# Kernel optimization log

Measured on AMD Instinct MI355X. Metric: run time of the kernel, lower is better.

The kernel has to match this reference:

```python
import jax, jax.numpy as jnp
import numpy as np

N, D, K = 32768, 256, 8192
SQRT3 = 3.0 ** 0.5


def setup_inputs() -> dict:
    key = jax.random.key(0)
    k1, k2 = jax.random.split(key)
    x = jax.random.normal(k1, (N, D), dtype=jnp.float32)
    # torch .uniform_(-sqrt(3), sqrt(3)) on an [D, K] table
    embeddings = jax.random.uniform(k2, (D, K), dtype=jnp.float32,
                                    minval=-SQRT3, maxval=SQRT3)
    return {"x": x, "embeddings": embeddings}


def reference(x, embeddings):
    # x: [N, D] (forward flattens from dim 1; 2D input is identity)
    # embeddings: [D, K]
    # squared L2 distances: ||y||^2 - 2 y.E + ||e||^2  -> [N, K]
    dist = (jnp.sum(x * x, axis=1, keepdims=True)
            - 2.0 * (x @ embeddings)
            + jnp.sum(embeddings * embeddings, axis=0, keepdims=True))
    idx = jnp.argmin(dist, axis=1)  # [N]
    # one_hot(idx) @ E^T == gather of columns of E (same math, no dense one-hot)
    quantized = jnp.take(embeddings, idx, axis=1).T  # [N, D]
    return quantized.reshape(x.shape)
```

## Files before the change

kernel.cpp:

```cpp
#include <hip/hip_runtime.h>
#include <math.h>
#include <float.h>

#define N_ROWS 32768
#define D_DIM  256
#define K_DIM  8192

#define EPS1 0.25f
#define EPS2 0.02f
#define T2CAP 4096
#define T3CAP 512
#define NSPLIT3 16

typedef _Float16 f16;
typedef _Float16 f16x8 __attribute__((ext_vector_type(8)));
typedef float f32x4 __attribute__((ext_vector_type(4)));

#define KSPLIT 8
#define COLS_PER_SPLIT (K_DIM / KSPLIT)
#define CHUNK_COLS 32
#define NCHUNK (COLS_PER_SPLIT / CHUNK_COLS)
#define CHUNK_BYTES (CHUNK_COLS * D_DIM * 2)

typedef unsigned int u32;
typedef const u32 __attribute__((address_space(1)))* gas1_u32;
typedef u32 __attribute__((address_space(3)))* las3_u32;
__device__ __forceinline__ void gload_lds16(const void* g, void* l) {
    __builtin_amdgcn_global_load_lds((gas1_u32)g, (las3_u32)l, 16, 0, 0);
}

__global__ void convx_kernel(const float* __restrict__ X, f16* __restrict__ X16) {
    const size_t i = ((size_t)blockIdx.x * 256 + threadIdx.x) * 8;
    float4 a = *reinterpret_cast<const float4*>(X + i);
    float4 b = *reinterpret_cast<const float4*>(X + i + 4);
    f16x8 o;
    o[0]=(f16)a.x; o[1]=(f16)a.y; o[2]=(f16)a.z; o[3]=(f16)a.w;
    o[4]=(f16)b.x; o[5]=(f16)b.y; o[6]=(f16)b.z; o[7]=(f16)b.w;
    *reinterpret_cast<f16x8*>(X16 + i) = o;
}

__global__ void transpose_kernel(const float* __restrict__ E, float* __restrict__ ET) {
    __shared__ float t[64][65];
    const int bk = blockIdx.x & (K_DIM / 64 - 1);
    const int bd = blockIdx.x >> 7;
    const int c  = threadIdx.x & 63;
    const int r0 = (threadIdx.x >> 6) * 16;
    const int d0 = bd * 64, k0 = bk * 64;
#pragma unroll
    for (int i = 0; i < 16; ++i)
        t[r0 + i][c] = E[(size_t)(d0 + r0 + i) * K_DIM + k0 + c];
    __syncthreads();
#pragma unroll
    for (int i = 0; i < 16; ++i)
        ET[(size_t)(k0 + r0 + i) * D_DIM + d0 + c] = t[c][r0 + i];
}

__global__ void packe_et_kernel(const float* __restrict__ ET, f16* __restrict__ Epack) {
    const int gid = blockIdx.x * 256 + threadIdx.x;
    const int l    = gid & 63;
    const int t    = (gid >> 6) & 7;
    const int tile = gid >> 9;
    const int k  = 16 * tile + (l & 15);
    const int d0 = 32 * t + (l >> 4) * 8;
    float4 a = *reinterpret_cast<const float4*>(&ET[(size_t)k * D_DIM + d0]);
    float4 b = *reinterpret_cast<const float4*>(&ET[(size_t)k * D_DIM + d0 + 4]);
    f16x8 o;
    o[0]=(f16)a.x; o[1]=(f16)a.y; o[2]=(f16)a.z; o[3]=(f16)a.w;
    o[4]=(f16)b.x; o[5]=(f16)b.y; o[6]=(f16)b.z; o[7]=(f16)b.w;
    *reinterpret_cast<f16x8*>(Epack + (size_t)gid * 8) = o;
}

__global__ void packe_kernel(const float* __restrict__ E, f16* __restrict__ Epack) {
    const int gid = blockIdx.x * 256 + threadIdx.x;
    const int l    = gid & 63;
    const int t    = (gid >> 6) & 7;
    const int tile = gid >> 9;
    const int k  = 16 * tile + (l & 15);
    const int d0 = 32 * t + (l >> 4) * 8;
    f16x8 o;
#pragma unroll
    for (int j = 0; j < 8; ++j) o[j] = (f16)E[(size_t)(d0 + j) * K_DIM + k];
    *reinterpret_cast<f16x8*>(Epack + (size_t)gid * 8) = o;
}

__global__ void nhen_kernel(const float* __restrict__ E, float* __restrict__ nhen) {
    const int k = blockIdx.x * 256 + threadIdx.x;
    float s = 0.0f;
#pragma unroll 8
    for (int d = 0; d < D_DIM; ++d) {
        float v = E[(size_t)d * K_DIM + k];
        s = fmaf(v, v, s);
    }
    nhen[k] = -0.5f * s;
}

__launch_bounds__(256, 2)
__global__ void pass1_kernel(const f16* __restrict__ X16,
                             const f16* __restrict__ Epack,
                             const float* __restrict__ nhen,
                             float* __restrict__ p_best,
                             float* __restrict__ p_sec,
                             int*   __restrict__ p_idx) {
    __shared__ f16 B_lds[3][CHUNK_BYTES / 2];
    __shared__ float nh_lds[COLS_PER_SPLIT];

    const int tid = threadIdx.x;
    const int wv = tid >> 6;
    const int lane = tid & 63;
    const int l15 = lane & 15;
    const int l4  = lane >> 4;
    const int rg = blockIdx.x >> 3;
    const int ks = blockIdx.x & 7;
    const int rowW = rg * 256 + wv * 64;
    const int colBase = ks * COLS_PER_SPLIT;

    f16x8 A[4][8];
#pragma unroll
    for (int rt = 0; rt < 4; ++rt)
#pragma unroll
        for (int t = 0; t < 8; ++t)
            A[rt][t] = *reinterpret_cast<const f16x8*>(
                X16 + (size_t)(rowW + 16*rt + l15) * D_DIM + 32*t + l4*8);

    *reinterpret_cast<float4*>(&nh_lds[tid * 4]) =
        *reinterpret_cast<const float4*>(nhen + colBase + tid * 4);

    float best[16], sec[16];
    int bbase[16];
#pragma unroll
    for (int s = 0; s < 16; ++s) { best[s] = -INFINITY; sec[s] = -INFINITY; bbase[s] = 0; }

    const char* splitSrc = (const char*)Epack + (size_t)colBase * 512;

    auto STAGE = [&](int buf, int ci) {
        const char* csrc = splitSrc + (size_t)ci * CHUNK_BYTES;
        char* cdst = (char*)&B_lds[buf][0];
#pragma unroll
        for (int c = 0; c < 4; ++c) {
            const int seg = wv * 4 + c;
            gload_lds16(csrc + seg * 1024 + (lane << 4), cdst + seg * 1024);
        }
    };

    f32x4 accA[4], accB[4];
    int cA = 0, cB = 0;

    auto TILE = [&](const f16* bufc, int ct, int nhoff,
                    f32x4 (&accN)[4], f32x4 (&accP)[4], int cP, bool doScore) {
        const float nh = nh_lds[nhoff + l15];
        const f32x4 nh4 = {nh, nh, nh, nh};
#pragma unroll
        for (int t = 0; t < 8; ++t) {
            f16x8 B = *reinterpret_cast<const f16x8*>(bufc + (ct*8 + t)*512 + lane*8);
            if (t == 0) {
#pragma unroll
                for (int rt = 0; rt < 4; ++rt)
                    accN[rt] = __builtin_amdgcn_mfma_f32_16x16x32_f16(A[rt][0], B, nh4, 0, 0, 0);
            } else {
#pragma unroll
                for (int rt = 0; rt < 4; ++rt)
                    accN[rt] = __builtin_amdgcn_mfma_f32_16x16x32_f16(A[rt][t], B, accN[rt], 0, 0, 0);
            }
            if (doScore) {
#pragma unroll
                for (int s = 2*t; s <= 2*t + 1; ++s) {
                    const int rt2 = s >> 2, r2 = s & 3;
                    const float v = accP[rt2][r2];
                    sec[s] = __builtin_amdgcn_fmed3f(v, best[s], sec[s]);
                    const bool gt = v > best[s];
                    best[s] = gt ? v : best[s];
                    bbase[s] = gt ? cP : bbase[s];
                }
            }
        }
    };

    STAGE(0, 0);
    STAGE(1, 1);
    asm volatile("s_waitcnt lgkmcnt(0)" ::: "memory");

    int cur = 0;
    for (int ci = 0; ci < NCHUNK; ++ci) {
        if (ci < NCHUNK - 1) {
            asm volatile("s_waitcnt vmcnt(4)" ::: "memory");
        } else {
            asm volatile("s_waitcnt vmcnt(0)" ::: "memory");
        }
        __builtin_amdgcn_s_barrier();
        if (ci + 2 < NCHUNK) {
            int nb = cur + 2; if (nb >= 3) nb -= 3;
            STAGE(nb, ci + 2);
        }
        const f16* bufc = &B_lds[cur][0];
        const int base = colBase + ci * CHUNK_COLS;
        if (ci == 0) {
            TILE(bufc, 0, ci*32,      accA, accB, cB, false); cA = base;
            TILE(bufc, 1, ci*32 + 16, accB, accA, cA, true);  cB = base + 16;
        } else {
            TILE(bufc, 0, ci*32,      accA, accB, cB, true);  cA = base;
            TILE(bufc, 1, ci*32 + 16, accB, accA, cA, true);  cB = base + 16;
        }
        cur = (cur + 1 == 3) ? 0 : cur + 1;
    }
#pragma unroll
    for (int s = 0; s < 16; ++s) {
        const int rt2 = s >> 2, r2 = s & 3;
        const float v = accB[rt2][r2];
        sec[s] = __builtin_amdgcn_fmed3f(v, best[s], sec[s]);
        const bool gt = v > best[s];
        best[s] = gt ? v : best[s];
        bbase[s] = gt ? cB : bbase[s];
    }

#pragma unroll
    for (int s = 0; s < 16; ++s) {
        float b = best[s], sc = sec[s];
        int k = bbase[s] + l15;
#pragma unroll
        for (int off = 8; off >= 1; off >>= 1) {
            float ob = __shfl_xor(b, off, 16);
            float os = __shfl_xor(sc, off, 16);
            int   ok = __shfl_xor(k, off, 16);
            float sm = fmaxf(fmaxf(sc, os), fminf(b, ob));
            bool take = (ob > b) || (ob == b && ok < k);
            b = take ? ob : b;
            k = take ? ok : k;
            sc = sm;
        }
        if (l15 == 0) {
            const int row = rowW + 16*(s >> 2) + 4*l4 + (s & 3);
            p_best[ks * N_ROWS + row] = b;
            p_sec [ks * N_ROWS + row] = sc;
            p_idx [ks * N_ROWS + row] = k;
        }
    }
}

__global__ void zero_counts_kernel(int* count, int* count3) { *count = 0; *count3 = 0; }

__global__ void merge_kernel(const float* __restrict__ p_best,
                             const float* __restrict__ p_sec,
                             const int*   __restrict__ p_idx,
                             int* __restrict__ idxf,
                             int* __restrict__ list, int* __restrict__ count) {
    const int n = blockIdx.x * 256 + threadIdx.x;
    float b = p_best[n], sc = p_sec[n];
    int k = p_idx[n];
#pragma unroll
    for (int s = 1; s < KSPLIT; ++s) {
        float ob = p_best[s * N_ROWS + n];
        float os = p_sec [s * N_ROWS + n];
        int   ok = p_idx [s * N_ROWS + n];
        float sm = fmaxf(fmaxf(sc, os), fminf(b, ob));
        bool take = ob > b;
        b = take ? ob : b; k = take ? ok : k; sc = sm;
    }
    idxf[n] = k;
    if (2.0f * (b - sc) < EPS1) {
        int pos = atomicAdd(count, 1);
        if (pos < T2CAP) list[pos] = n;
    }
}

__launch_bounds__(256, 2)
__global__ void tier2_kernel(const float* __restrict__ X,
                             const float* __restrict__ E,
                             const float* __restrict__ nhen,
                             const int* __restrict__ list,
                             const int* __restrict__ count,
                             float* __restrict__ t2b, float* __restrict__ t2s,
                             int* __restrict__ t2i) {
    const int g  = blockIdx.x >> 4;
    const int sp = blockIdx.x & 15;
    const int cnt = min(*count, T2CAP);
    if (g * 64 >= cnt) return;

    __shared__ float xT[D_DIM][64];
    __shared__ float es[64][64];
    const int tid = threadIdx.x;
    const int tx = tid & 15, ty = tid >> 4;

    {
        const int r = tid >> 2;
        const int slot = min(g * 64 + r, cnt - 1);
        const int row = list[slot];
        const int d0 = (tid & 3) * 64;
        const float* xp = X + (size_t)row * D_DIM + d0;
#pragma unroll
        for (int i = 0; i < 64; i += 4) {
            float4 v = *reinterpret_cast<const float4*>(xp + i);
            xT[d0+i+0][r] = v.x; xT[d0+i+1][r] = v.y;
            xT[d0+i+2][r] = v.z; xT[d0+i+3][r] = v.w;
        }
    }

    float best[4], sec[4]; int bidx[4];
#pragma unroll
    for (int i = 0; i < 4; ++i) { best[i] = -INFINITY; sec[i] = -INFINITY; bidx[i] = 0; }

    const int colBase = sp * 512;
    for (int kc = 0; kc < 512; kc += 64) {
        float acc[4][4];
#pragma unroll
        for (int i = 0; i < 4; ++i)
#pragma unroll
            for (int j = 0; j < 4; ++j) acc[i][j] = 0.0f;

        for (int dc = 0; dc < D_DIM; dc += 64) {
            __syncthreads();
#pragma unroll
            for (int dd = 0; dd < 64; dd += 16) {
                int d = dd + (tid >> 4);
                float4 v = *reinterpret_cast<const float4*>(
                    &E[(size_t)(dc + d) * K_DIM + colBase + kc + (tid & 15) * 4]);
                *reinterpret_cast<float4*>(&es[d][(tid & 15) * 4]) = v;
            }
            __syncthreads();
#pragma unroll 8
            for (int d = 0; d < 64; ++d) {
                float4 xv = *reinterpret_cast<const float4*>(&xT[dc + d][ty * 4]);
                float4 ev = *reinterpret_cast<const float4*>(&es[d][tx * 4]);
                float xr[4] = {xv.x, xv.y, xv.z, xv.w};
                float ec[4] = {ev.x, ev.y, ev.z, ev.w};
#pragma unroll
                for (int i = 0; i < 4; ++i)
#pragma unroll
                    for (int j = 0; j < 4; ++j)
                        acc[i][j] = fmaf(xr[i], ec[j], acc[i][j]);
            }
        }
        float4 nhv = *reinterpret_cast<const float4*>(&nhen[colBase + kc + tx * 4]);
        float nh[4] = {nhv.x, nhv.y, nhv.z, nhv.w};
#pragma unroll
        for (int j = 0; j < 4; ++j) {
            const int k = colBase + kc + tx * 4 + j;
#pragma unroll
            for (int i = 0; i < 4; ++i) {
                float u = nh[j] + acc[i][j];
                bool gt = u > best[i];
                sec[i]  = fmaxf(sec[i], fminf(u, best[i]));
                best[i] = gt ? u : best[i];
                bidx[i] = gt ? k : bidx[i];
            }
        }
    }

#pragma unroll
    for (int off = 8; off >= 1; off >>= 1) {
#pragma unroll
        for (int i = 0; i < 4; ++i) {
            float ob = __shfl_xor(best[i], off, 16);
            float os = __shfl_xor(sec[i], off, 16);
            int   ok = __shfl_xor(bidx[i], off, 16);
            float sm = fmaxf(fmaxf(sec[i], os), fminf(best[i], ob));
            bool take = (ob > best[i]) || (ob == best[i] && ok < bidx[i]);
            best[i] = take ? ob : best[i];
            bidx[i] = take ? ok : bidx[i];
            sec[i] = sm;
        }
    }
    if (tx == 0) {
#pragma unroll
        for (int i = 0; i < 4; ++i) {
            const int slot = g * 64 + ty * 4 + i;
            if (slot < cnt) {
                t2b[sp * T2CAP + slot] = best[i];
                t2s[sp * T2CAP + slot] = sec[i];
                t2i[sp * T2CAP + slot] = bidx[i];
            }
        }
    }
}

__global__ void merge2_kernel(const float* __restrict__ t2b,
                              const float* __restrict__ t2s,
                              const int*   __restrict__ t2i,
                              const int* __restrict__ list,
                              const int* __restrict__ count,
                              int* __restrict__ idxf,
                              int* __restrict__ list3, int* __restrict__ count3) {
    const int slot = blockIdx.x * 256 + threadIdx.x;
    const int cnt = min(*count, T2CAP);
    if (slot >= cnt) return;
    float b = t2b[slot], sc = t2s[slot];
    int k = t2i[slot];
#pragma unroll
    for (int sp = 1; sp < 16; ++sp) {
        float ob = t2b[sp * T2CAP + slot];
        float os = t2s[sp * T2CAP + slot];
        int   ok = t2i[sp * T2CAP + slot];
        float sm = fmaxf(fmaxf(sc, os), fminf(b, ob));
        bool take = ob > b;
        b = take ? ob : b; k = take ? ok : k; sc = sm;
    }
    const int n = list[slot];
    idxf[n] = k;
    if (2.0f * (b - sc) < EPS2) {
        int pos = atomicAdd(count3, 1);
        if (pos < T3CAP) list3[pos] = n;
    }
}

__launch_bounds__(256)
__global__ void tier3_kernel(const float* __restrict__ X,
                             const float* __restrict__ E,
                             const int* __restrict__ list3,
                             const int* __restrict__ count3,
                             double* __restrict__ t3b, int* __restrict__ t3i) {
    const int slot = blockIdx.x >> 4;
    const int sp   = blockIdx.x & 15;
    const int cnt = min(*count3, T3CAP);
    if (slot >= cnt) return;
    const int n = list3[slot];

    __shared__ float xs[D_DIM];
    const int tid = threadIdx.x;
    xs[tid] = X[(size_t)n * D_DIM + tid];
    __syncthreads();

    const int colBase = sp * 512;
    double best = DBL_MAX;
    int bi = 0x7fffffff;
#pragma unroll
    for (int kk = 0; kk < 512; kk += 256) {
        const int k = colBase + kk + tid;
        double s0 = 0.0, s1 = 0.0, s2 = 0.0, s3 = 0.0;
#pragma unroll 4
        for (int d = 0; d < D_DIM; d += 4) {
            double f0 = (double)xs[d+0] - (double)E[(size_t)(d+0) * K_DIM + k];
            double f1 = (double)xs[d+1] - (double)E[(size_t)(d+1) * K_DIM + k];
            double f2 = (double)xs[d+2] - (double)E[(size_t)(d+2) * K_DIM + k];
            double f3 = (double)xs[d+3] - (double)E[(size_t)(d+3) * K_DIM + k];
            s0 = fma(f0, f0, s0); s1 = fma(f1, f1, s1);
            s2 = fma(f2, f2, s2); s3 = fma(f3, f3, s3);
        }
        double s = (s0 + s1) + (s2 + s3);
        if (s < best) { best = s; bi = k; }
    }

    __shared__ double bv[256];
    __shared__ int bix[256];
    bv[tid] = best; bix[tid] = bi;
    __syncthreads();
    if (tid == 0) {
        double b = bv[0]; int ix = bix[0];
        for (int t = 1; t < 256; ++t)
            if (bv[t] < b || (bv[t] == b && bix[t] < ix)) { b = bv[t]; ix = bix[t]; }
        t3b[sp * T3CAP + slot] = b;
        t3i[sp * T3CAP + slot] = ix;
    }
}

__global__ void merge3_kernel(const double* __restrict__ t3b,
                              const int* __restrict__ t3i,
                              const int* __restrict__ list3,
                              const int* __restrict__ count3,
                              int* __restrict__ idxf) {
    const int slot = blockIdx.x * 256 + threadIdx.x;
    const int cnt = min(*count3, T3CAP);
    if (slot >= cnt) return;
    double b = t3b[slot];
    int k = t3i[slot];
#pragma unroll
    for (int sp = 1; sp < NSPLIT3; ++sp) {
        double ob = t3b[sp * T3CAP + slot];
        int   ok = t3i[sp * T3CAP + slot];
        if (ob < b || (ob == b && ok < k)) { b = ob; k = ok; }
    }
    idxf[list3[slot]] = k;
}

__global__ void gather2_kernel(const float* __restrict__ ET,
                               const int* __restrict__ idx,
                               float* __restrict__ out) {
    const int n  = blockIdx.x * 4 + (threadIdx.x >> 6);
    const int d4 = (threadIdx.x & 63) * 4;
    const int k  = idx[n];
    *reinterpret_cast<float4*>(&out[(size_t)n * D_DIM + d4]) =
        *reinterpret_cast<const float4*>(&ET[(size_t)k * D_DIM + d4]);
}

__global__ void gather_kernel(const float* __restrict__ E,
                              const int* __restrict__ idx,
                              float* __restrict__ out) {
    const int n = blockIdx.x;
    const int d = threadIdx.x;
    const int k = idx[n];
    out[(size_t)n * D_DIM + d] = E[(size_t)d * K_DIM + k];
}

__global__ void fb_enorm_kernel(const float* __restrict__ E, float* __restrict__ enorm) {
    int k = blockIdx.x * 256 + threadIdx.x;
    float s = 0.0f;
#pragma unroll 8
    for (int d = 0; d < D_DIM; ++d) { float v = E[(size_t)d * K_DIM + k]; s = fmaf(v, v, s); }
    enorm[k] = s;
}

__launch_bounds__(256, 2)
__global__ void fb_dist_kernel(const float* __restrict__ X, const float* __restrict__ E,
                               const float* __restrict__ enorm,
                               int* __restrict__ idx_out, float* __restrict__ gap_out) {
    __shared__ float xT[D_DIM][64];
    __shared__ float es[64][64];
    const int tid = threadIdx.x;
    const int tx = tid & 15, ty = tid >> 4;
    const int rowBase = blockIdx.x * 64;
    {
        const int r = tid >> 2;
        const int d0 = (tid & 3) * 64;
        const float* xp = X + (size_t)(rowBase + r) * D_DIM + d0;
#pragma unroll
        for (int i = 0; i < 64; i += 4) {
            float4 v = *reinterpret_cast<const float4*>(xp + i);
            xT[d0+i+0][r]=v.x; xT[d0+i+1][r]=v.y; xT[d0+i+2][r]=v.z; xT[d0+i+3][r]=v.w;
        }
    }
    float bestVal[4], secVal[4]; int bestIdx[4];
#pragma unroll
    for (int i = 0; i < 4; ++i) { bestVal[i]=INFINITY; secVal[i]=INFINITY; bestIdx[i]=0; }
    for (int kc = 0; kc < K_DIM; kc += 64) {
        float acc[4][4];
#pragma unroll
        for (int i=0;i<4;++i)
#pragma unroll
            for (int j=0;j<4;++j) acc[i][j]=0.f;
        for (int dc = 0; dc < D_DIM; dc += 64) {
            __syncthreads();
#pragma unroll
            for (int dd = 0; dd < 64; dd += 16) {
                int d = dd + (tid >> 4);
                float4 v = *reinterpret_cast<const float4*>(
                    &E[(size_t)(dc+d)*K_DIM + kc + (tid&15)*4]);
                *reinterpret_cast<float4*>(&es[d][(tid&15)*4]) = v;
            }
            __syncthreads();
#pragma unroll 8
            for (int d = 0; d < 64; ++d) {
                float4 xv = *reinterpret_cast<const float4*>(&xT[dc+d][ty*4]);
                float4 ev = *reinterpret_cast<const float4*>(&es[d][tx*4]);
                float xr[4]={xv.x,xv.y,xv.z,xv.w}, ec[4]={ev.x,ev.y,ev.z,ev.w};
#pragma unroll
                for (int i=0;i<4;++i)
#pragma unroll
                    for (int j=0;j<4;++j) acc[i][j]=fmaf(xr[i],ec[j],acc[i][j]);
            }
        }
        float4 env = *reinterpret_cast<const float4*>(&enorm[kc + tx*4]);
        float en[4]={env.x,env.y,env.z,env.w};
#pragma unroll
        for (int j=0;j<4;++j) {
            int k = kc + tx*4 + j;
#pragma unroll
            for (int i=0;i<4;++i) {
                float s = fmaf(-2.0f, acc[i][j], en[j]);
                if (s < bestVal[i]) { secVal[i]=bestVal[i]; bestVal[i]=s; bestIdx[i]=k; }
                else if (s < secVal[i]) secVal[i]=s;
            }
        }
    }
#pragma unroll
    for (int off=8; off>=1; off>>=1) {
#pragma unroll
        for (int i=0;i<4;++i) {
            float oB=__shfl_xor(bestVal[i],off,16);
            int oI=__shfl_xor(bestIdx[i],off,16);
            float oS=__shfl_xor(secVal[i],off,16);
            float ms=fminf(fminf(secVal[i],oS),fmaxf(bestVal[i],oB));
            if (oB<bestVal[i] || (oB==bestVal[i] && oI<bestIdx[i])) { bestVal[i]=oB; bestIdx[i]=oI; }
            secVal[i]=ms;
        }
    }
    if (tx==0) {
#pragma unroll
        for (int i=0;i<4;++i) {
            idx_out[rowBase + ty*4 + i] = bestIdx[i];
            gap_out[rowBase + ty*4 + i] = secVal[i]-bestVal[i];
        }
    }
}

__launch_bounds__(256)
__global__ void fb_refine_kernel(const float* __restrict__ X, const float* __restrict__ E,
                                 const float* __restrict__ gap, int* __restrict__ idx) {
    const int n = blockIdx.x;
    if (gap[n] >= 0.0625f) return;
    __shared__ float xs[D_DIM];
    const int tid = threadIdx.x;
    xs[tid] = X[(size_t)n * D_DIM + tid];
    __syncthreads();
    double best = DBL_MAX; int bi = 0x7fffffff;
    for (int k = tid; k < K_DIM; k += 256) {
        double s0=0,s1=0,s2=0,s3=0;
#pragma unroll 4
        for (int d = 0; d < D_DIM; d += 4) {
            double f0=(double)xs[d+0]-(double)E[(size_t)(d+0)*K_DIM+k];
            double f1=(double)xs[d+1]-(double)E[(size_t)(d+1)*K_DIM+k];
            double f2=(double)xs[d+2]-(double)E[(size_t)(d+2)*K_DIM+k];
            double f3=(double)xs[d+3]-(double)E[(size_t)(d+3)*K_DIM+k];
            s0=fma(f0,f0,s0); s1=fma(f1,f1,s1); s2=fma(f2,f2,s2); s3=fma(f3,f3,s3);
        }
        double s=(s0+s1)+(s2+s3);
        if (s<best){best=s;bi=k;}
    }
    __shared__ double bv[256]; __shared__ int bix[256];
    bv[tid]=best; bix[tid]=bi;
    __syncthreads();
    if (tid==0) {
        double b=bv[0]; int ix=bix[0];
        for (int t=1;t<256;++t)
            if (bv[t]<b || (bv[t]==b && bix[t]<ix)) { b=bv[t]; ix=bix[t]; }
        idx[n]=ix;
    }
}

extern "C" void kernel_launch(void* const* d_in, const int* in_sizes, int n_in,
                              void* d_out, int out_size, void* d_ws, size_t ws_size,
                              hipStream_t stream) {
    const float* X = (const float*)d_in[0];
    const float* E = (const float*)d_in[1];
    float* out = (float*)d_out;
    char* ws = (char*)d_ws;

    const size_t o_nhen  = 0;
    const size_t o_pb    = 32768;
    const size_t o_ps    = o_pb  + (size_t)KSPLIT * N_ROWS * 4;
    const size_t o_pi    = o_ps  + (size_t)KSPLIT * N_ROWS * 4;
    const size_t o_idx   = o_pi  + (size_t)KSPLIT * N_ROWS * 4;
    const size_t o_list  = o_idx + (size_t)N_ROWS * 4;
    const size_t o_count = o_list + (size_t)T2CAP * 4;
    const size_t o_t2b   = o_count + 256;
    const size_t o_t2s   = o_t2b + (size_t)16 * T2CAP * 4;
    const size_t o_t2i   = o_t2s + (size_t)16 * T2CAP * 4;
    const size_t o_list3 = o_t2i + (size_t)16 * T2CAP * 4;
    const size_t o_t3b   = o_list3 + (size_t)T3CAP * 4;
    const size_t o_t3i   = o_t3b + (size_t)NSPLIT3 * T3CAP * 8;
    const size_t o_x16   = o_t3i + (size_t)NSPLIT3 * T3CAP * 4;
    const size_t o_epack = o_x16 + (size_t)N_ROWS * D_DIM * 2;
    const size_t NEED_BASE = o_epack + (size_t)D_DIM * K_DIM * 2;
    const size_t o_et    = NEED_BASE;
    const size_t NEED_FULL = o_et + (size_t)D_DIM * K_DIM * 4;

    if (ws_size >= NEED_BASE) {
        float*  nhen  = (float*) (ws + o_nhen);
        float*  p_b   = (float*) (ws + o_pb);
        float*  p_s   = (float*) (ws + o_ps);
        int*    p_i   = (int*)   (ws + o_pi);
        int*    idxf  = (int*)   (ws + o_idx);
        int*    list  = (int*)   (ws + o_list);
        int*    count = (int*)   (ws + o_count);
        int*    count3= (int*)   (ws + o_count + 4);
        float*  t2b   = (float*) (ws + o_t2b);
        float*  t2s   = (float*) (ws + o_t2s);
        int*    t2i   = (int*)   (ws + o_t2i);
        int*    list3 = (int*)   (ws + o_list3);
        double* t3b   = (double*)(ws + o_t3b);
        int*    t3i   = (int*)   (ws + o_t3i);
        f16*    X16   = (f16*)   (ws + o_x16);
        f16*    Epack = (f16*)   (ws + o_epack);
        float*  ET    = (float*) (ws + o_et);
        const bool haveET = ws_size >= NEED_FULL;

        convx_kernel<<<(N_ROWS * D_DIM / 8) / 256, 256, 0, stream>>>(X, X16);
        if (haveET) {
            transpose_kernel<<<(K_DIM / 64) * (D_DIM / 64), 256, 0, stream>>>(E, ET);
            packe_et_kernel<<<(K_DIM / 16) * 8 * 64 / 256, 256, 0, stream>>>(ET, Epack);
        } else {
            packe_kernel<<<(K_DIM / 16) * 8 * 64 / 256, 256, 0, stream>>>(E, Epack);
        }
        nhen_kernel<<<K_DIM / 256, 256, 0, stream>>>(E, nhen);
        zero_counts_kernel<<<1, 1, 0, stream>>>(count, count3);
        pass1_kernel<<<(N_ROWS / 256) * KSPLIT, 256, 0, stream>>>(
            X16, Epack, nhen, p_b, p_s, p_i);
        merge_kernel<<<N_ROWS / 256, 256, 0, stream>>>(
            p_b, p_s, p_i, idxf, list, count);
        tier2_kernel<<<(T2CAP / 64) * 16, 256, 0, stream>>>(
            X, E, nhen, list, count, t2b, t2s, t2i);
        merge2_kernel<<<T2CAP / 256, 256, 0, stream>>>(
            t2b, t2s, t2i, list, count, idxf, list3, count3);
        tier3_kernel<<<T3CAP * NSPLIT3, 256, 0, stream>>>(
            X, E, list3, count3, t3b, t3i);
        merge3_kernel<<<T3CAP / 256, 256, 0, stream>>>(
            t3b, t3i, list3, count3, idxf);
        if (haveET)
            gather2_kernel<<<N_ROWS / 4, 256, 0, stream>>>(ET, idxf, out);
        else
            gather_kernel<<<N_ROWS, 256, 0, stream>>>(E, idxf, out);
    } else {
        float* enorm = (float*)ws;
        int*   idx   = (int*)(ws + 32768);
        float* gap   = (float*)(ws + 32768 + (size_t)N_ROWS * 4);
        fb_enorm_kernel<<<K_DIM / 256, 256, 0, stream>>>(E, enorm);
        fb_dist_kernel<<<N_ROWS / 64, 256, 0, stream>>>(X, E, enorm, idx, gap);
        fb_refine_kernel<<<N_ROWS, 256, 0, stream>>>(X, E, gap, idx);
        gather_kernel<<<N_ROWS, 256, 0, stream>>>(E, idx, out);
    }
}
```

Baseline: 324.3 us.

## Fuse E transpose with fp16 packing, fold count reset, split tier2 wider

The transpose kernel now also emits the packed fp16 fragment layout straight from its shared-memory tile, so the separate pack kernel and its re-read of ET are gone. Resetting the atomic counters moves into the X conversion kernel, which removes one tiny launch. Tier-2 refinement splits the codebook into 32 column ranges instead of 16 to launch more blocks, at the cost of twice as many partial results for merge2 to reduce.

```diff
diff --git a/kernel.cpp b/kernel.cpp
--- a/kernel.cpp
+++ b/kernel.cpp
@@ -9,6 +9,7 @@
 #define EPS1 0.25f
 #define EPS2 0.02f
 #define T2CAP 4096
+#define NSPLIT2 32
 #define T3CAP 512
 #define NSPLIT3 16
 
@@ -29,7 +30,9 @@
     __builtin_amdgcn_global_load_lds((gas1_u32)g, (las3_u32)l, 16, 0, 0);
 }
 
-__global__ void convx_kernel(const float* __restrict__ X, f16* __restrict__ X16) {
+__global__ void convx_kernel(const float* __restrict__ X, f16* __restrict__ X16,
+                             int* __restrict__ count, int* __restrict__ count3) {
+    if (blockIdx.x == 0 && threadIdx.x == 0) { *count = 0; *count3 = 0; }
     const size_t i = ((size_t)blockIdx.x * 256 + threadIdx.x) * 8;
     float4 a = *reinterpret_cast<const float4*>(X + i);
     float4 b = *reinterpret_cast<const float4*>(X + i + 4);
@@ -39,7 +42,8 @@
     *reinterpret_cast<f16x8*>(X16 + i) = o;
 }
 
-__global__ void transpose_kernel(const float* __restrict__ E, float* __restrict__ ET) {
+__global__ void prep_e_kernel(const float* __restrict__ E, float* __restrict__ ET,
+                              f16* __restrict__ Epack) {
     __shared__ float t[64][65];
     const int bk = blockIdx.x & (K_DIM / 64 - 1);
     const int bd = blockIdx.x >> 7;
@@ -53,21 +57,20 @@
 #pragma unroll
     for (int i = 0; i < 16; ++i)
         ET[(size_t)(k0 + r0 + i) * D_DIM + d0 + c] = t[c][r0 + i];
-}
-
-__global__ void packe_et_kernel(const float* __restrict__ ET, f16* __restrict__ Epack) {
-    const int gid = blockIdx.x * 256 + threadIdx.x;
-    const int l    = gid & 63;
-    const int t    = (gid >> 6) & 7;
-    const int tile = gid >> 9;
-    const int k  = 16 * tile + (l & 15);
-    const int d0 = 32 * t + (l >> 4) * 8;
-    float4 a = *reinterpret_cast<const float4*>(&ET[(size_t)k * D_DIM + d0]);
-    float4 b = *reinterpret_cast<const float4*>(&ET[(size_t)k * D_DIM + d0 + 4]);
-    f16x8 o;
-    o[0]=(f16)a.x; o[1]=(f16)a.y; o[2]=(f16)a.z; o[3]=(f16)a.w;
-    o[4]=(f16)b.x; o[5]=(f16)b.y; o[6]=(f16)b.z; o[7]=(f16)b.w;
-    *reinterpret_cast<f16x8*>(Epack + (size_t)gid * 8) = o;
+#pragma unroll
+    for (int o = 0; o < 2; ++o) {
+        const int out = threadIdx.x + o * 256;
+        const int i16 = out >> 7;
+        const int th  = (out >> 6) & 1;
+        const int l   = out & 63;
+        const int tile = bk * 4 + i16;
+        const int tg   = bd * 2 + th;
+        f16x8 frag;
+#pragma unroll
+        for (int j = 0; j < 8; ++j)
+            frag[j] = (f16)t[32*th + (l >> 4) * 8 + j][16*i16 + (l & 15)];
+        *reinterpret_cast<f16x8*>(Epack + ((size_t)(tile*8 + tg) * 512 + l * 8)) = frag;
+    }
 }
 
 __global__ void packe_kernel(const float* __restrict__ E, f16* __restrict__ Epack) {
@@ -236,8 +239,6 @@
     }
 }
 
-__global__ void zero_counts_kernel(int* count, int* count3) { *count = 0; *count3 = 0; }
-
 __global__ void merge_kernel(const float* __restrict__ p_best,
                              const float* __restrict__ p_sec,
                              const int*   __restrict__ p_idx,
@@ -270,8 +271,8 @@
                              const int* __restrict__ count,
                              float* __restrict__ t2b, float* __restrict__ t2s,
                              int* __restrict__ t2i) {
-    const int g  = blockIdx.x >> 4;
-    const int sp = blockIdx.x & 15;
+    const int g  = blockIdx.x >> 5;
+    const int sp = blockIdx.x & 31;
     const int cnt = min(*count, T2CAP);
     if (g * 64 >= cnt) return;
 
@@ -298,8 +299,8 @@
 #pragma unroll
     for (int i = 0; i < 4; ++i) { best[i] = -INFINITY; sec[i] = -INFINITY; bidx[i] = 0; }
 
-    const int colBase = sp * 512;
-    for (int kc = 0; kc < 512; kc += 64) {
+    const int colBase = sp * 256;
+    for (int kc = 0; kc < 256; kc += 64) {
         float acc[4][4];
 #pragma unroll
         for (int i = 0; i < 4; ++i)
@@ -385,7 +386,7 @@
     float b = t2b[slot], sc = t2s[slot];
     int k = t2i[slot];
 #pragma unroll
-    for (int sp = 1; sp < 16; ++sp) {
+    for (int sp = 1; sp < NSPLIT2; ++sp) {
         float ob = t2b[sp * T2CAP + slot];
         float os = t2s[sp * T2CAP + slot];
         int   ok = t2i[sp * T2CAP + slot];
@@ -630,9 +631,9 @@
     const size_t o_list  = o_idx + (size_t)N_ROWS * 4;
     const size_t o_count = o_list + (size_t)T2CAP * 4;
     const size_t o_t2b   = o_count + 256;
-    const size_t o_t2s   = o_t2b + (size_t)16 * T2CAP * 4;
-    const size_t o_t2i   = o_t2s + (size_t)16 * T2CAP * 4;
-    const size_t o_list3 = o_t2i + (size_t)16 * T2CAP * 4;
+    const size_t o_t2s   = o_t2b + (size_t)NSPLIT2 * T2CAP * 4;
+    const size_t o_t2i   = o_t2s + (size_t)NSPLIT2 * T2CAP * 4;
+    const size_t o_list3 = o_t2i + (size_t)NSPLIT2 * T2CAP * 4;
     const size_t o_t3b   = o_list3 + (size_t)T3CAP * 4;
     const size_t o_t3i   = o_t3b + (size_t)NSPLIT3 * T3CAP * 8;
     const size_t o_x16   = o_t3i + (size_t)NSPLIT3 * T3CAP * 4;
@@ -661,20 +662,18 @@
         float*  ET    = (float*) (ws + o_et);
         const bool haveET = ws_size >= NEED_FULL;
 
-        convx_kernel<<<(N_ROWS * D_DIM / 8) / 256, 256, 0, stream>>>(X, X16);
+        convx_kernel<<<(N_ROWS * D_DIM / 8) / 256, 256, 0, stream>>>(X, X16, count, count3);
         if (haveET) {
-            transpose_kernel<<<(K_DIM / 64) * (D_DIM / 64), 256, 0, stream>>>(E, ET);
-            packe_et_kernel<<<(K_DIM / 16) * 8 * 64 / 256, 256, 0, stream>>>(ET, Epack);
+            prep_e_kernel<<<(K_DIM / 64) * (D_DIM / 64), 256, 0, stream>>>(E, ET, Epack);
         } else {
             packe_kernel<<<(K_DIM / 16) * 8 * 64 / 256, 256, 0, stream>>>(E, Epack);
         }
         nhen_kernel<<<K_DIM / 256, 256, 0, stream>>>(E, nhen);
-        zero_counts_kernel<<<1, 1, 0, stream>>>(count, count3);
         pass1_kernel<<<(N_ROWS / 256) * KSPLIT, 256, 0, stream>>>(
             X16, Epack, nhen, p_b, p_s, p_i);
         merge_kernel<<<N_ROWS / 256, 256, 0, stream>>>(
             p_b, p_s, p_i, idxf, list, count);
-        tier2_kernel<<<(T2CAP / 64) * 16, 256, 0, stream>>>(
+        tier2_kernel<<<(T2CAP / 64) * NSPLIT2, 256, 0, stream>>>(
             X, E, nhen, list, count, t2b, t2s, t2i);
         merge2_kernel<<<T2CAP / 256, 256, 0, stream>>>(
             t2b, t2s, t2i, list, count, idxf, list3, count3);
```

After: 310.7 us. 4.2% less time.
